# Performance work log

Measured on AMD Instinct MI355X. Metric: run time of the kernel, lower is better.

The kernel has to match this reference:

```python
import jax, jax.numpy as jnp
import numpy as np

F_SIZE = 1024
N_HEADS = 16
HEAD = F_SIZE // N_HEADS
EPS = 1e-5


def setup_inputs() -> dict:
    key = jax.random.key(0)
    ks = jax.random.split(key, 8)
    B, N, F = 4, 1024, F_SIZE
    in_feats = jax.random.normal(ks[0], (B, N, F), dtype=jnp.float32)
    pos_feats = jax.random.normal(ks[1], (B, N, F), dtype=jnp.float32)
    # parameters (torch Linear convention: W [out, in], y = x @ W.T + b)
    xav = lambda k, o, i: jax.random.uniform(k, (o, i), jnp.float32, -1.0, 1.0) * np.sqrt(6.0 / (o + i))
    ln_g = jnp.ones((F,), jnp.float32)
    ln_b = jnp.zeros((F,), jnp.float32)
    w_qk = xav(ks[2], 2 * F, F)
    b_qk = jnp.zeros((2 * F,), jnp.float32)
    w_v = xav(ks[3], F, F)
    b_v = jnp.zeros((F,), jnp.float32)
    w_o = xav(ks[4], F, F)
    b_o = jnp.zeros((F,), jnp.float32)
    return {"in_feats": in_feats, "pos_feats": pos_feats, "ln_g": ln_g, "ln_b": ln_b,
            "w_qk": w_qk, "b_qk": b_qk, "w_v": w_v, "b_v": b_v, "w_o": w_o, "b_o": b_o}


def reference(in_feats, pos_feats, ln_g, ln_b, w_qk, b_qk, w_v, b_v, w_o, b_o):
    B, N, F = in_feats.shape
    H, D = N_HEADS, HEAD
    # LayerNorm (biased variance, eps=1e-5 as torch default)
    mu = jnp.mean(in_feats, axis=-1, keepdims=True)
    var = jnp.mean(jnp.square(in_feats - mu), axis=-1, keepdims=True)
    norm = (in_feats - mu) * jax.lax.rsqrt(var + EPS) * ln_g + ln_b
    pos_norm = norm + pos_feats
    # QK projection on pos-added features, V projection on norm features
    qk = pos_norm @ w_qk.T + b_qk                      # [B,N,2F]
    q = qk[..., :F].reshape(B, N, H, D)
    k = qk[..., F:].reshape(B, N, H, D)
    v = (norm @ w_v.T + b_v).reshape(B, N, H, D)
    scale = float(D) ** -0.5
    scores = jnp.einsum('bnhd,bmhd->bhnm', q, k) * scale
    attn = jax.nn.softmax(scores, axis=-1)
    wv = jnp.einsum('bhnm,bmhd->bnhd', attn, v).reshape(B, N, F)
    delta = wv @ w_o.T + b_o
    return in_feats + delta
```

## Files before the change

### kernel.cpp

```cpp
#include <hip/hip_runtime.h>
#include <hip/hip_bf16.h>
#include <stdint.h>

#define FDIM 1024
#define NHEADS 16
#define HDIM 64
#define BATCH 4
#define SEQ 1024
#define MROWS (BATCH*SEQ)

typedef short bf16x8 __attribute__((ext_vector_type(8)));
typedef float f32x4 __attribute__((ext_vector_type(4)));

__device__ inline unsigned short f2bf(float f){
  union { float f; uint32_t u; } v; v.f = f;
  uint32_t u = v.u;
  uint32_t r = (u + 0x7fffu + ((u >> 16) & 1u)) >> 16;
  return (unsigned short)r;
}

__device__ inline void gld_lds16(const void* g, void* l){
  __builtin_amdgcn_global_load_lds((const __attribute__((address_space(1))) uint32_t*)g,
                                   (__attribute__((address_space(3))) uint32_t*)l, 16, 0, 0);
}

__global__ __launch_bounds__(256) void cvt_w(const float* __restrict__ src,
                                             unsigned short* __restrict__ dst, int n4){
  int i = blockIdx.x*256 + threadIdx.x;
  if (i < n4){
    float4 v = ((const float4*)src)[i];
    ushort4 o; o.x=f2bf(v.x); o.y=f2bf(v.y); o.z=f2bf(v.z); o.w=f2bf(v.w);
    ((ushort4*)dst)[i] = o;
  }
}

__global__ __launch_bounds__(256) void ln_posadd(const float* __restrict__ x,
                                                 const float* __restrict__ pos,
                                                 const float* __restrict__ g,
                                                 const float* __restrict__ be,
                                                 unsigned short* __restrict__ normb,
                                                 unsigned short* __restrict__ posnb){
  int row = blockIdx.x, t = threadIdx.x;
  float4 v = ((const float4*)(x + (size_t)row*FDIM))[t];
  float s  = v.x+v.y+v.z+v.w;
  float sq = v.x*v.x+v.y*v.y+v.z*v.z+v.w*v.w;
  #pragma unroll
  for (int off=32; off>=1; off>>=1){ s += __shfl_down(s,off); sq += __shfl_down(sq,off); }
  __shared__ float red[8];
  int w=t>>6, lane=t&63;
  if (!lane){ red[w]=s; red[4+w]=sq; }
  __syncthreads();
  s  = red[0]+red[1]+red[2]+red[3];
  sq = red[4]+red[5]+red[6]+red[7];
  float mu  = s*(1.0f/FDIM);
  float var = sq*(1.0f/FDIM) - mu*mu;
  float rs  = rsqrtf(var + 1e-5f);
  float4 gg=((const float4*)g)[t], bb=((const float4*)be)[t];
  float4 pp=((const float4*)(pos + (size_t)row*FDIM))[t];
  float n0=(v.x-mu)*rs*gg.x+bb.x, n1=(v.y-mu)*rs*gg.y+bb.y;
  float n2=(v.z-mu)*rs*gg.z+bb.z, n3=(v.w-mu)*rs*gg.w+bb.w;
  ushort4 nb; nb.x=f2bf(n0); nb.y=f2bf(n1); nb.z=f2bf(n2); nb.w=f2bf(n3);
  ushort4 pb; pb.x=f2bf(n0+pp.x); pb.y=f2bf(n1+pp.y); pb.z=f2bf(n2+pp.z); pb.w=f2bf(n3+pp.w);
  ((ushort4*)(normb+(size_t)row*FDIM))[t]=nb;
  ((ushort4*)(posnb+(size_t)row*FDIM))[t]=pb;
}

template<int MODE>
__global__ __launch_bounds__(256) void gemm_bt(const unsigned short* __restrict__ A,
                                               const unsigned short* __restrict__ Bw,
                                               const float* __restrict__ bias,
                                               const float* __restrict__ resid,
                                               void* __restrict__ Cout,
                                               int M, int Nout, int K){
  __shared__ unsigned short Als[128*32];
  __shared__ unsigned short Bls[128*32];
  int t = threadIdx.x, w = t>>6, lane = t&63;
  int m0 = blockIdx.x*128, n0 = blockIdx.y*128;
  int wm = (w>>1)*64, wn = (w&1)*64;
  int lrow = lane&15, lk = (lane>>4)*8, rg = lane>>4;
  f32x4 acc[4][4] = {};
  for (int k0=0; k0<K; k0+=32){
    #pragma unroll
    for (int i=0;i<2;i++){
      int c = t + i*256;
      gld_lds16(A  + (size_t)(m0 + (c>>2))*K + k0 + (c&3)*8, Als + c*8);
      gld_lds16(Bw + (size_t)(n0 + (c>>2))*K + k0 + (c&3)*8, Bls + c*8);
    }
    __syncthreads();
    bf16x8 a[4], b[4];
    #pragma unroll
    for (int i=0;i<4;i++){
      a[i] = *(const bf16x8*)&Als[(wm + i*16 + lrow)*32 + lk];
      b[i] = *(const bf16x8*)&Bls[(wn + i*16 + lrow)*32 + lk];
    }
    #pragma unroll
    for (int mi=0;mi<4;mi++)
      #pragma unroll
      for (int ni=0;ni<4;ni++)
        acc[mi][ni] = __builtin_amdgcn_mfma_f32_16x16x32_bf16(a[mi], b[ni], acc[mi][ni], 0,0,0);
    __syncthreads();
  }
  #pragma unroll
  for (int mi=0;mi<4;mi++){
    #pragma unroll
    for (int ni=0;ni<4;ni++){
      int n = n0 + wn + ni*16 + lrow;
      float bs = bias[n];
      #pragma unroll
      for (int r=0;r<4;r++){
        int m = m0 + wm + mi*16 + rg*4 + r;
        float vv = acc[mi][ni][r] + bs;
        size_t idx = (size_t)m*Nout + n;
        if (MODE==0) ((unsigned short*)Cout)[idx] = f2bf(vv);
        else         ((float*)Cout)[idx] = vv + resid[idx];
      }
    }
  }
}

__global__ __launch_bounds__(256) void attn(const unsigned short* __restrict__ qk,
                                            const unsigned short* __restrict__ vbuf,
                                            unsigned short* __restrict__ wvbuf){
  __shared__ unsigned short Qls[64*64];
  __shared__ unsigned short Kls[64*64];
  __shared__ unsigned short Vtls[64*64];
  __shared__ unsigned short Pls[64*64];
  int t=threadIdx.x, w=t>>6, lane=t&63;
  int lrow=lane&15, lk=(lane>>4)*8, rg=lane>>4;
  int q0=blockIdx.x*64, h=blockIdx.y, b=blockIdx.z;
  const size_t qs = 2*FDIM;
  #pragma unroll
  for (int i=0;i<2;i++){
    int c=t+i*256;
    gld_lds16(qk + (size_t)(b*SEQ + q0 + (c>>3))*qs + h*HDIM + (c&7)*8, Qls + c*8);
  }
  f32x4 o[4] = {};
  float m_run[4], l_run[4];
  #pragma unroll
  for (int r=0;r<4;r++){ m_run[r]=-1e30f; l_run[r]=0.f; }
  __syncthreads();
  bf16x8 qa[2];
  qa[0] = *(const bf16x8*)&Qls[(w*16+lrow)*64 + lk];
  qa[1] = *(const bf16x8*)&Qls[(w*16+lrow)*64 + 32 + lk];

  for (int kt=0; kt<16; ++kt){
    int key0 = kt*64;
    __syncthreads();
    #pragma unroll
    for (int i=0;i<2;i++){
      int c=t+i*256;
      gld_lds16(qk + (size_t)(b*SEQ + key0 + (c>>3))*qs + FDIM + h*HDIM + (c&7)*8, Kls + c*8);
    }
    #pragma unroll
    for (int i=0;i<2;i++){
      int c=t+i*256;
      int key=c&63, d0=(c>>6)*8;
      bf16x8 vv = *(const bf16x8*)(vbuf + (size_t)(b*SEQ + key0 + key)*FDIM + h*HDIM + d0);
      #pragma unroll
      for (int j=0;j<8;j++) Vtls[(d0+j)*64 + key] = (unsigned short)vv[j];
    }
    __syncthreads();
    f32x4 s[4] = {};
    #pragma unroll
    for (int kf=0; kf<2; kf++){
      #pragma unroll
      for (int ni=0;ni<4;ni++){
        bf16x8 kb = *(const bf16x8*)&Kls[(ni*16+lrow)*64 + kf*32 + lk];
        s[ni] = __builtin_amdgcn_mfma_f32_16x16x32_bf16(qa[kf], kb, s[ni], 0,0,0);
      }
    }
    #pragma unroll
    for (int r=0;r<4;r++){
      float tm = fmaxf(fmaxf(s[0][r],s[1][r]), fmaxf(s[2][r],s[3][r])) * 0.125f;
      #pragma unroll
      for (int off=1; off<16; off<<=1) tm = fmaxf(tm, __shfl_xor(tm, off));
      float mn = fmaxf(m_run[r], tm);
      float sc = __expf(m_run[r] - mn);
      float p[4]; float ts = 0.f;
      #pragma unroll
      for (int ni=0;ni<4;ni++){ p[ni] = __expf(s[ni][r]*0.125f - mn); ts += p[ni]; }
      #pragma unroll
      for (int off=1; off<16; off<<=1) ts += __shfl_xor(ts, off);
      l_run[r] = l_run[r]*sc + ts;
      m_run[r] = mn;
      #pragma unroll
      for (int nd=0;nd<4;nd++) o[nd][r] *= sc;
      #pragma unroll
      for (int ni=0;ni<4;ni++) Pls[(w*16 + rg*4 + r)*64 + ni*16 + lrow] = f2bf(p[ni]);
    }
    asm volatile("s_waitcnt lgkmcnt(0)" ::: "memory");
    #pragma unroll
    for (int kf=0; kf<2; kf++){
      bf16x8 pa = *(const bf16x8*)&Pls[(w*16+lrow)*64 + kf*32 + lk];
      #pragma unroll
      for (int nd=0;nd<4;nd++){
        bf16x8 vb = *(const bf16x8*)&Vtls[(nd*16+lrow)*64 + kf*32 + lk];
        o[nd] = __builtin_amdgcn_mfma_f32_16x16x32_bf16(pa, vb, o[nd], 0,0,0);
      }
    }
  }
  #pragma unroll
  for (int nd=0; nd<4; nd++){
    #pragma unroll
    for (int r=0;r<4;r++){
      float val = o[nd][r] / l_run[r];
      wvbuf[(size_t)(b*SEQ + q0 + w*16 + rg*4 + r)*FDIM + h*HDIM + nd*16 + lrow] = f2bf(val);
    }
  }
}

extern "C" void kernel_launch(void* const* d_in, const int* in_sizes, int n_in,
                              void* d_out, int out_size, void* d_ws, size_t ws_size,
                              hipStream_t stream) {
  const float* in_feats = (const float*)d_in[0];
  const float* pos      = (const float*)d_in[1];
  const float* ln_g     = (const float*)d_in[2];
  const float* ln_b     = (const float*)d_in[3];
  const float* w_qk     = (const float*)d_in[4];
  const float* b_qk     = (const float*)d_in[5];
  const float* w_v      = (const float*)d_in[6];
  const float* b_v      = (const float*)d_in[7];
  const float* w_o      = (const float*)d_in[8];
  const float* b_o      = (const float*)d_in[9];
  float* out = (float*)d_out;

  char* ws = (char*)d_ws;
  unsigned short* norm_b = (unsigned short*)(ws + 0);
  unsigned short* posn_b = (unsigned short*)(ws + (8u<<20));
  unsigned short* wqk_b  = (unsigned short*)(ws + (16u<<20));
  unsigned short* wv_b   = (unsigned short*)(ws + (20u<<20));
  unsigned short* wo_b   = (unsigned short*)(ws + (22u<<20));
  unsigned short* qk_buf = (unsigned short*)(ws + (24u<<20));
  unsigned short* v_buf  = (unsigned short*)(ws + (40u<<20));
  unsigned short* wv_out = norm_b;

  cvt_w<<<(2048*1024/4 + 255)/256, 256, 0, stream>>>(w_qk, wqk_b, 2048*1024/4);
  cvt_w<<<(1024*1024/4 + 255)/256, 256, 0, stream>>>(w_v,  wv_b,  1024*1024/4);
  cvt_w<<<(1024*1024/4 + 255)/256, 256, 0, stream>>>(w_o,  wo_b,  1024*1024/4);
  ln_posadd<<<MROWS, 256, 0, stream>>>(in_feats, pos, ln_g, ln_b, norm_b, posn_b);
  gemm_bt<0><<<dim3(MROWS/128, 2048/128), 256, 0, stream>>>(posn_b, wqk_b, b_qk, nullptr,
                                                            qk_buf, MROWS, 2048, FDIM);
  gemm_bt<0><<<dim3(MROWS/128, 1024/128), 256, 0, stream>>>(norm_b, wv_b, b_v, nullptr,
                                                            v_buf, MROWS, 1024, FDIM);
  attn<<<dim3(SEQ/64, NHEADS, BATCH), 256, 0, stream>>>(qk_buf, v_buf, wv_out);
  gemm_bt<1><<<dim3(MROWS/128, 1024/128), 256, 0, stream>>>(wv_out, wo_b, b_o, in_feats,
                                                            out, MROWS, 1024, FDIM);
}
```

Measured before the change: 275.5 us.

## Swizzle attention LDS tiles, remap blocks for XCD locality, use exp2 softmax

The attention kernel now stores its Q, K, transposed-V and P tiles in LDS with an XOR swizzle on 16-byte column groups, to remove the bank conflicts caused by the 128-byte row stride during MFMA operand reads and the scattered transposes. The 3D grid is flattened into a 1D grid with a block-index remap so that blocks sharing a head and batch, which reuse the same K/V, are grouped onto the same XCD for better L2 reuse. Softmax folds log2(e) into the scale and uses exp2f, and the explicit lgkmcnt wait is dropped on the assumption that in-order LDS access within a wave is enough. The swizzle adds some index arithmetic, and the remap assumes round-robin dispatch of blocks across eight XCDs.

```diff
diff --git a/kernel.cpp b/kernel.cpp
--- a/kernel.cpp
+++ b/kernel.cpp
@@ -22,6 +22,10 @@
 __device__ inline void gld_lds16(const void* g, void* l){
   __builtin_amdgcn_global_load_lds((const __attribute__((address_space(1))) uint32_t*)g,
                                    (__attribute__((address_space(3))) uint32_t*)l, 16, 0, 0);
+}
+
+__device__ inline bf16x8 ldsw(const unsigned short* base, int row, int colgrp){
+  return *(const bf16x8*)&base[row*64 + (((colgrp) ^ (row&7))<<3)];
 }
 
 __global__ __launch_bounds__(256) void cvt_w(const float* __restrict__ src,
@@ -126,13 +130,15 @@
   __shared__ unsigned short Vtls[64*64];
   __shared__ unsigned short Pls[64*64];
   int t=threadIdx.x, w=t>>6, lane=t&63;
-  int lrow=lane&15, lk=(lane>>4)*8, rg=lane>>4;
-  int q0=blockIdx.x*64, h=blockIdx.y, b=blockIdx.z;
+  int lrow=lane&15, lcg=lane>>4, rg=lane>>4;
+  int bid = blockIdx.x;
+  int wgid = (bid&7)*128 + (bid>>3);
+  int q0 = (wgid&15)*64, h = (wgid>>4)&15, b = wgid>>8;
   const size_t qs = 2*FDIM;
   #pragma unroll
   for (int i=0;i<2;i++){
-    int c=t+i*256;
-    gld_lds16(qk + (size_t)(b*SEQ + q0 + (c>>3))*qs + h*HDIM + (c&7)*8, Qls + c*8);
+    int c=t+i*256, row=c>>3, cg=(c&7)^(row&7);
+    gld_lds16(qk + (size_t)(b*SEQ + q0 + row)*qs + h*HDIM + cg*8, Qls + c*8);
   }
   f32x4 o[4] = {};
   float m_run[4], l_run[4];
@@ -140,16 +146,18 @@
   for (int r=0;r<4;r++){ m_run[r]=-1e30f; l_run[r]=0.f; }
   __syncthreads();
   bf16x8 qa[2];
-  qa[0] = *(const bf16x8*)&Qls[(w*16+lrow)*64 + lk];
-  qa[1] = *(const bf16x8*)&Qls[(w*16+lrow)*64 + 32 + lk];
+  qa[0] = ldsw(Qls, w*16+lrow, 0*4 + lcg);
+  qa[1] = ldsw(Qls, w*16+lrow, 1*4 + lcg);
+
+  const float SCL = 0.125f * 1.44269504f;
 
   for (int kt=0; kt<16; ++kt){
     int key0 = kt*64;
     __syncthreads();
     #pragma unroll
     for (int i=0;i<2;i++){
-      int c=t+i*256;
-      gld_lds16(qk + (size_t)(b*SEQ + key0 + (c>>3))*qs + FDIM + h*HDIM + (c&7)*8, Kls + c*8);
+      int c=t+i*256, row=c>>3, cg=(c&7)^(row&7);
+      gld_lds16(qk + (size_t)(b*SEQ + key0 + row)*qs + FDIM + h*HDIM + cg*8, Kls + c*8);
     }
     #pragma unroll
     for (int i=0;i<2;i++){
@@ -157,7 +165,8 @@
       int key=c&63, d0=(c>>6)*8;
       bf16x8 vv = *(const bf16x8*)(vbuf + (size_t)(b*SEQ + key0 + key)*FDIM + h*HDIM + d0);
       #pragma unroll
-      for (int j=0;j<8;j++) Vtls[(d0+j)*64 + key] = (unsigned short)vv[j];
+      for (int j=0;j<8;j++)
+        Vtls[(d0+j)*64 + ((((key>>3) ^ j))<<3) + (key&7)] = (unsigned short)vv[j];
     }
     __syncthreads();
     f32x4 s[4] = {};
@@ -165,36 +174,37 @@
     for (int kf=0; kf<2; kf++){
       #pragma unroll
       for (int ni=0;ni<4;ni++){
-        bf16x8 kb = *(const bf16x8*)&Kls[(ni*16+lrow)*64 + kf*32 + lk];
+        bf16x8 kb = ldsw(Kls, ni*16+lrow, kf*4 + lcg);
         s[ni] = __builtin_amdgcn_mfma_f32_16x16x32_bf16(qa[kf], kb, s[ni], 0,0,0);
       }
     }
     #pragma unroll
     for (int r=0;r<4;r++){
-      float tm = fmaxf(fmaxf(s[0][r],s[1][r]), fmaxf(s[2][r],s[3][r])) * 0.125f;
+      float tm = fmaxf(fmaxf(s[0][r],s[1][r]), fmaxf(s[2][r],s[3][r])) * SCL;
       #pragma unroll
       for (int off=1; off<16; off<<=1) tm = fmaxf(tm, __shfl_xor(tm, off));
       float mn = fmaxf(m_run[r], tm);
-      float sc = __expf(m_run[r] - mn);
+      float sc = exp2f(m_run[r] - mn);
       float p[4]; float ts = 0.f;
       #pragma unroll
-      for (int ni=0;ni<4;ni++){ p[ni] = __expf(s[ni][r]*0.125f - mn); ts += p[ni]; }
+      for (int ni=0;ni<4;ni++){ p[ni] = exp2f(s[ni][r]*SCL - mn); ts += p[ni]; }
       #pragma unroll
       for (int off=1; off<16; off<<=1) ts += __shfl_xor(ts, off);
       l_run[r] = l_run[r]*sc + ts;
       m_run[r] = mn;
       #pragma unroll
       for (int nd=0;nd<4;nd++) o[nd][r] *= sc;
-      #pragma unroll
-      for (int ni=0;ni<4;ni++) Pls[(w*16 + rg*4 + r)*64 + ni*16 + lrow] = f2bf(p[ni]);
-    }
-    asm volatile("s_waitcnt lgkmcnt(0)" ::: "memory");
+      int pr = w*16 + rg*4 + r;
+      #pragma unroll
+      for (int ni=0;ni<4;ni++)
+        Pls[pr*64 + (((ni*2 + (lrow>>3)) ^ (pr&7))<<3) + (lrow&7)] = f2bf(p[ni]);
+    }
     #pragma unroll
     for (int kf=0; kf<2; kf++){
-      bf16x8 pa = *(const bf16x8*)&Pls[(w*16+lrow)*64 + kf*32 + lk];
+      bf16x8 pa = ldsw(Pls, w*16+lrow, kf*4 + lcg);
       #pragma unroll
       for (int nd=0;nd<4;nd++){
-        bf16x8 vb = *(const bf16x8*)&Vtls[(nd*16+lrow)*64 + kf*32 + lk];
+        bf16x8 vb = ldsw(Vtls, nd*16+lrow, kf*4 + lcg);
         o[nd] = __builtin_amdgcn_mfma_f32_16x16x32_bf16(pa, vb, o[nd], 0,0,0);
       }
     }
@@ -242,7 +252,7 @@
                                                             qk_buf, MROWS, 2048, FDIM);
   gemm_bt<0><<<dim3(MROWS/128, 1024/128), 256, 0, stream>>>(norm_b, wv_b, b_v, nullptr,
                                                             v_buf, MROWS, 1024, FDIM);
-  attn<<<dim3(SEQ/64, NHEADS, BATCH), 256, 0, stream>>>(qk_buf, v_buf, wv_out);
+  attn<<<dim3(SEQ/64 * NHEADS * BATCH), 256, 0, stream>>>(qk_buf, v_buf, wv_out);
   gemm_bt<1><<<dim3(MROWS/128, 1024/128), 256, 0, stream>>>(wv_out, wo_b, b_o, in_feats,
                                                             out, MROWS, 1024, FDIM);
 }
```

Measured after the change: 268.8 us. 2.4% less time.
